# Kernel tuning notes

Hardware: AMD Instinct MI355X
Metric: run time of the kernel (lower is better)

Reference implementation:

```python
import jax, jax.numpy as jnp
import numpy as np

EMBED = 1024
HEADS = 16
HEAD_DIM = EMBED // HEADS
SCALE = HEAD_DIM ** -0.5


def setup_inputs() -> dict:
    key = jax.random.key(0)
    ks = jax.random.split(key, 11)
    B, S, D = 2, 2048, EMBED
    s = D ** -0.5
    return {
        "Q": jax.random.normal(ks[0], (B, S, D), jnp.float32),
        "K": jax.random.normal(ks[1], (B, S, D), jnp.float32),
        "V": jax.random.normal(ks[2], (B, S, D), jnp.float32),
        "Wq": jax.random.normal(ks[3], (D, D), jnp.float32) * s,
        "bq": jax.random.normal(ks[4], (D,), jnp.float32) * 0.01,
        "Wk": jax.random.normal(ks[5], (D, D), jnp.float32) * s,
        "bk": jax.random.normal(ks[6], (D,), jnp.float32) * 0.01,
        "Wv": jax.random.normal(ks[7], (D, D), jnp.float32) * s,
        "bv": jax.random.normal(ks[8], (D,), jnp.float32) * 0.01,
        "Wo": jax.random.normal(ks[9], (D, D), jnp.float32) * s,
        "bo": jax.random.normal(ks[10], (D,), jnp.float32) * 0.01,
    }


def reference(Q, K, V, Wq, bq, Wk, bk, Wv, bv, Wo, bo):
    N, S, D = Q.shape
    H, Hd = HEADS, HEAD_DIM
    # linear projections (x @ W + b), then split heads: [N, S, H, Hd]
    q = (Q @ Wq + bq).reshape(N, S, H, Hd)
    k = (K @ Wk + bk).reshape(N, S, H, Hd)
    v = (V @ Wv + bv).reshape(N, S, H, Hd)
    # scaled dot-product attention, full [N,H,S,S] scores as in the original
    energy = jnp.einsum('nqhd,nkhd->nhqk', q, k) * SCALE
    attn = jax.nn.softmax(energy, axis=3)
    out = jnp.einsum('nhql,nlhd->nqhd', attn, v).reshape(N, S, D)
    return out @ Wo + bo
```

## Files before the change

kernel.cpp:

```cpp
#include <hip/hip_runtime.h>
#include <cstdint>


typedef _Float16 h8 __attribute__((ext_vector_type(8)));
typedef float f4 __attribute__((ext_vector_type(4)));
typedef float f16v __attribute__((ext_vector_type(16)));
typedef unsigned int u32x4 __attribute__((ext_vector_type(4)));
typedef const unsigned int __attribute__((address_space(1)))* gp1_t;
typedef unsigned int __attribute__((address_space(3)))* lp3_t;

__device__ __forceinline__ void gld_lds16(const void* g, const void* l) {
  __builtin_amdgcn_global_load_lds((gp1_t)(uintptr_t)g,
                                   (lp3_t)(unsigned int)(uintptr_t)l, 16, 0, 0);
}
__device__ __forceinline__ unsigned pkh(float a, float b) {
  return __builtin_bit_cast(unsigned, __builtin_amdgcn_cvt_pkrtz(a, b));
}
__device__ __forceinline__ void plswap(unsigned& a, unsigned& b) {
  asm volatile("v_permlane32_swap_b32 %0, %1" : "+v"(a), "+v"(b));
}


__global__ void cvt_x3(const float* __restrict__ a, const float* __restrict__ b,
                       const float* __restrict__ c, _Float16* __restrict__ out) {
  const int z = blockIdx.z;
  const float* in = (z == 0) ? a : (z == 1) ? b : c;
  _Float16* o = out + (size_t)z * 4194304;
  const int i = (blockIdx.x * 256 + threadIdx.x) * 8;
  float4 u = *(const float4*)(in + i);
  float4 w = *(const float4*)(in + i + 4);
  h8 r = {(_Float16)u.x, (_Float16)u.y, (_Float16)u.z, (_Float16)u.w,
          (_Float16)w.x, (_Float16)w.y, (_Float16)w.z, (_Float16)w.w};
  *(h8*)(o + i) = r;
}

__global__ void cvt_w4(const float* __restrict__ wq, const float* __restrict__ wk,
                       const float* __restrict__ wv, const float* __restrict__ wo,
                       _Float16* __restrict__ WT) {
  const int z = blockIdx.z;
  const float* W = (z == 0) ? wq : (z == 1) ? wk : (z == 2) ? wv : wo;
  _Float16* o = WT + (size_t)z * 1048576;
  const int k = blockIdx.x * 256 + threadIdx.x;
  const int n0 = blockIdx.y * 4;
  float4 w = *(const float4*)(W + (size_t)k * 1024 + n0);
  o[(size_t)(n0 + 0) * 1024 + k] = (_Float16)w.x;
  o[(size_t)(n0 + 1) * 1024 + k] = (_Float16)w.y;
  o[(size_t)(n0 + 2) * 1024 + k] = (_Float16)w.z;
  o[(size_t)(n0 + 3) * 1024 + k] = (_Float16)w.w;
}


__device__ __forceinline__ void gemm_core(const _Float16* __restrict__ A,
                                          const _Float16* __restrict__ Bt,
                                          const float* __restrict__ bias,
                                          _Float16* __restrict__ out16,
                                          float* __restrict__ out32,
                                          int N, int K, int mode) {
  __shared__ _Float16 As[8192];
  __shared__ _Float16 Bs[8192];
  const int tid = threadIdx.x;
  const int wave = tid >> 6, lane = tid & 63;
  const int lg = lane >> 4, ll = lane & 15;
  const int wr = wave >> 1, wc = wave & 1;
  const int row0 = blockIdx.y * 128, col0 = blockIdx.x * 128;
  f4 acc[4][4] = {};
  const int nkt = K >> 6;
  for (int kt = 0; kt < nkt; ++kt) {
#pragma unroll
    for (int rr = 0; rr < 4; ++rr) {
      const int idx = rr * 256 + tid;
      const int r = idx >> 3, g = idx & 7;
      const int lb = (rr * 256 + wave * 64) * 8;
      gld_lds16(A + (size_t)(row0 + r) * K + kt * 64 + g * 8, &As[lb]);
      gld_lds16(Bt + (size_t)(col0 + r) * K + kt * 64 + g * 8, &Bs[lb]);
    }
    __syncthreads();
#pragma unroll
    for (int kk = 0; kk < 2; ++kk) {
      h8 af[4], bf[4];
#pragma unroll
      for (int mi = 0; mi < 4; ++mi)
        af[mi] = *(const h8*)&As[(wr * 64 + mi * 16 + ll) * 64 + kk * 32 + lg * 8];
#pragma unroll
      for (int ni = 0; ni < 4; ++ni)
        bf[ni] = *(const h8*)&Bs[(wc * 64 + ni * 16 + ll) * 64 + kk * 32 + lg * 8];
#pragma unroll
      for (int mi = 0; mi < 4; ++mi)
#pragma unroll
        for (int ni = 0; ni < 4; ++ni)
          acc[mi][ni] = __builtin_amdgcn_mfma_f32_16x16x32_f16(af[mi], bf[ni],
                                                               acc[mi][ni], 0, 0, 0);
    }
    __syncthreads();
  }
#pragma unroll
  for (int ni = 0; ni < 4; ++ni) {
    const int c = col0 + wc * 64 + ni * 16 + ll;
    const float bv = bias[c];
#pragma unroll
    for (int mi = 0; mi < 4; ++mi) {
#pragma unroll
      for (int i = 0; i < 4; ++i) {
        const int r = row0 + wr * 64 + mi * 16 + lg * 4 + i;
        const float val = acc[mi][ni][i] + bv;
        if (mode == 0) {
          const int b = r >> 11, s = r & 2047, h = c >> 6, hd = c & 63;
          out16[((size_t)((b * 16 + h) * 2048 + s)) * 64 + hd] = (_Float16)val;
        } else {
          out32[(size_t)r * N + c] = val;
        }
      }
    }
  }
}

__global__ __launch_bounds__(256) void gemm_qkv(const _Float16* __restrict__ X16,
                                                const _Float16* __restrict__ WT,
                                                const float* __restrict__ bq,
                                                const float* __restrict__ bk,
                                                const float* __restrict__ bv,
                                                _Float16* __restrict__ qkv16) {
  const int z = blockIdx.z;
  gemm_core(X16 + (size_t)z * 4194304, WT + (size_t)z * 1048576,
            (z == 0) ? bq : (z == 1) ? bk : bv, qkv16 + (size_t)z * 4194304,
            nullptr, 1024, 1024, 0);
}

__global__ __launch_bounds__(256) void gemm_out_k(const _Float16* __restrict__ A16,
                                                  const _Float16* __restrict__ WoT,
                                                  const float* __restrict__ bo,
                                                  float* __restrict__ out) {
  gemm_core(A16, WoT, bo, nullptr, out, 1024, 1024, 1);
}


#define STAGE_K(BUF, KT)                                                      \
  do {                                                                        \
    _Pragma("unroll") for (int rr = 0; rr < 2; ++rr) {                        \
      const int idx_ = rr * 256 + tid;                                        \
      const int r_ = idx_ >> 3, g_ = idx_ & 7;                                \
      gld_lds16(kbp + (size_t)((KT) * 64 + r_) * 64 + ((g_ ^ (r_ & 7)) * 8),  \
                &Ks[BUF][rr * 2048 + wave * 512]);                            \
    }                                                                         \
  } while (0)

#define LOAD_V(KT, VA, VC)                                                    \
  do {                                                                        \
    const _Float16* vp_ = vbp + (size_t)((KT) * 64 + vkey0) * 64 + vhd0;      \
    VA = *(const uint4*)vp_;                                                  \
    VC = *(const uint4*)(vp_ + 64);                                           \
  } while (0)

#define WRITE_V(BUF, VA, VC)                                                  \
  do {                                                                        \
    const unsigned short* pa_ = (const unsigned short*)&VA;                   \
    const unsigned short* pc_ = (const unsigned short*)&VC;                   \
    _Pragma("unroll") for (int j_ = 0; j_ < 8; ++j_) {                        \
      const int row_ = vhd0 + j_;                                             \
      const int hi_ = row_ * 64 + (((vkey0 >> 3) ^ (row_ & 7)) << 3) + (vkey0 & 7); \
      *(unsigned int*)&Vt[BUF][hi_] =                                         \
          (unsigned)pa_[j_] | ((unsigned)pc_[j_] << 16);                      \
    }                                                                         \
  } while (0)

#define PV_STEP(SX, PP, KBP)                                                  \
  do {                                                                        \
    unsigned wA = pkh(SX[(PP) + 0], SX[(PP) + 1]);                            \
    unsigned wB = pkh(SX[(PP) + 2], SX[(PP) + 3]);                            \
    unsigned wC = pkh(SX[(PP) + 4], SX[(PP) + 5]);                            \
    unsigned wD = pkh(SX[(PP) + 6], SX[(PP) + 7]);                            \
    plswap(wA, wC);                                                           \
    plswap(wB, wD);                                                           \
    u32x4 afu = {wA, wB, wC, wD};                                             \
    h8 af = __builtin_bit_cast(h8, afu);                                      \
    const int sw_ = (((KBP) * 2 + hi) ^ (l31 & 7)) << 3;                      \
    h8 vf0 = *(const h8*)&Vt[cur][l31 * 64 + sw_];                            \
    h8 vf1 = *(const h8*)&Vt[cur][(32 + l31) * 64 + sw_];                     \
    acc0 = __builtin_amdgcn_mfma_f32_32x32x16_f16(af, vf0, acc0, 0, 0, 0);    \
    acc1 = __builtin_amdgcn_mfma_f32_32x32x16_f16(af, vf1, acc1, 0, 0, 0);    \
  } while (0)

__global__ __launch_bounds__(256, 2) void attn_kernel(
    const _Float16* __restrict__ q16, const _Float16* __restrict__ k16,
    const _Float16* __restrict__ v16, _Float16* __restrict__ aout) {
  __shared__ _Float16 Ks[2][4096];
  __shared__ _Float16 Vt[2][4096];
  __shared__ float Fb[4][32];
  const int tid = threadIdx.x;
  const int wave = tid >> 6, lane = tid & 63;
  const int l31 = lane & 31, hi = lane >> 5;
  const int bh = blockIdx.x, qb = blockIdx.y;
  const int q0w = qb * 128 + wave * 32;
  const _Float16* qbp = q16 + (size_t)bh * 131072;
  const _Float16* kbp = k16 + (size_t)bh * 131072;
  const _Float16* vbp = v16 + (size_t)bh * 131072;
  const int vkey0 = (tid & 31) * 2, vhd0 = (tid >> 5) * 8;

  h8 qf0 = *(const h8*)(qbp + (size_t)(q0w + l31) * 64 + 0 + hi * 8);
  h8 qf1 = *(const h8*)(qbp + (size_t)(q0w + l31) * 64 + 16 + hi * 8);
  h8 qf2 = *(const h8*)(qbp + (size_t)(q0w + l31) * 64 + 32 + hi * 8);
  h8 qf3 = *(const h8*)(qbp + (size_t)(q0w + l31) * 64 + 48 + hi * 8);

  f16v acc0 = {}, acc1 = {};
  float mval = -1e30f, lsum = 0.f;
  const float C = 0.125f * 1.44269504089f;

  {
    uint4 va, vc;
    STAGE_K(0, 0);
    LOAD_V(0, va, vc);
    WRITE_V(0, va, vc);
  }
  __syncthreads();

  int cur = 0;
  for (int kt = 0; kt < 32; ++kt) {
    uint4 va, vc;
    const bool pre = (kt + 1 < 32);
    if (pre) { STAGE_K(cur ^ 1, kt + 1); LOAD_V(kt + 1, va, vc); }

    f16v s0 = {}, s1 = {};
#pragma unroll
    for (int kc = 0; kc < 4; ++kc) {
      const int sw = ((kc * 2 + hi) ^ (l31 & 7)) << 3;
      h8 k0 = *(const h8*)&Ks[cur][l31 * 64 + sw];
      h8 k1 = *(const h8*)&Ks[cur][(32 + l31) * 64 + sw];
      h8 qf = (kc == 0) ? qf0 : (kc == 1) ? qf1 : (kc == 2) ? qf2 : qf3;
      s0 = __builtin_amdgcn_mfma_f32_32x32x16_f16(k0, qf, s0, 0, 0, 0);
      s1 = __builtin_amdgcn_mfma_f32_32x32x16_f16(k1, qf, s1, 0, 0, 0);
    }

    float t[8];
#pragma unroll
    for (int j = 0; j < 8; ++j)
      t[j] = fmaxf(fmaxf(s0[j], s0[j + 8]), fmaxf(s1[j], s1[j + 8]));
    float pm = fmaxf(fmaxf(fmaxf(t[0], t[1]), fmaxf(t[2], t[3])),
                     fmaxf(fmaxf(t[4], t[5]), fmaxf(t[6], t[7])));
    pm = fmaxf(pm, __shfl_xor(pm, 32));
    const float pms = pm * C;

    if (__any(pms > mval + 8.0f)) {
      const float mnew = fmaxf(mval, pms);
      const float f = __builtin_amdgcn_exp2f(mval - mnew);
      mval = mnew;
      lsum *= f;
      Fb[wave][l31] = f;
      const f4 fr0 = *(const f4*)&Fb[wave][0 + 4 * hi];
      const f4 fr1 = *(const f4*)&Fb[wave][8 + 4 * hi];
      const f4 fr2 = *(const f4*)&Fb[wave][16 + 4 * hi];
      const f4 fr3 = *(const f4*)&Fb[wave][24 + 4 * hi];
#pragma unroll
      for (int r = 0; r < 16; ++r) {
        const float fx = (r < 4 ? fr0 : r < 8 ? fr1 : r < 12 ? fr2 : fr3)[r & 3];
        acc0[r] *= fx;
        acc1[r] *= fx;
      }
    }

#pragma unroll
    for (int r = 0; r < 16; ++r) {
      s0[r] = __builtin_amdgcn_exp2f(s0[r] * C - mval);
      s1[r] = __builtin_amdgcn_exp2f(s1[r] * C - mval);
    }
    float z[8];
#pragma unroll
    for (int j = 0; j < 8; ++j)
      z[j] = (s0[j] + s0[j + 8]) + (s1[j] + s1[j + 8]);
    lsum += ((z[0] + z[1]) + (z[2] + z[3])) + ((z[4] + z[5]) + (z[6] + z[7]));

    PV_STEP(s0, 0, 0);
    PV_STEP(s0, 8, 1);
    PV_STEP(s1, 0, 2);
    PV_STEP(s1, 8, 3);

    if (pre) WRITE_V(cur ^ 1, va, vc);
    __syncthreads();
    cur ^= 1;
  }

  lsum += __shfl_xor(lsum, 32);
  const float inv = 1.0f / lsum;
  Fb[wave][l31] = inv;
  const f4 ir0 = *(const f4*)&Fb[wave][0 + 4 * hi];
  const f4 ir1 = *(const f4*)&Fb[wave][8 + 4 * hi];
  const f4 ir2 = *(const f4*)&Fb[wave][16 + 4 * hi];
  const f4 ir3 = *(const f4*)&Fb[wave][24 + 4 * hi];
  const int b = bh >> 4, h = bh & 15;
#pragma unroll
  for (int r = 0; r < 16; ++r) {
    const float fx = (r < 4 ? ir0 : r < 8 ? ir1 : r < 12 ? ir2 : ir3)[r & 3];
    const int srow = q0w + (r & 3) + 8 * (r >> 2) + 4 * hi;
    _Float16* op = aout + ((size_t)(b * 2048 + srow)) * 1024 + h * 64 + l31;
    op[0] = (_Float16)(acc0[r] * fx);
    op[32] = (_Float16)(acc1[r] * fx);
  }
}


extern "C" void kernel_launch(void* const* d_in, const int* in_sizes, int n_in,
                              void* d_out, int out_size, void* d_ws, size_t ws_size,
                              hipStream_t stream) {
  const float* Q  = (const float*)d_in[0];
  const float* K  = (const float*)d_in[1];
  const float* V  = (const float*)d_in[2];
  const float* Wq = (const float*)d_in[3];
  const float* bq = (const float*)d_in[4];
  const float* Wk = (const float*)d_in[5];
  const float* bk = (const float*)d_in[6];
  const float* Wv = (const float*)d_in[7];
  const float* bv = (const float*)d_in[8];
  const float* Wo = (const float*)d_in[9];
  const float* bo = (const float*)d_in[10];

  _Float16* H      = (_Float16*)d_ws;
  _Float16* X16    = H;
  _Float16* WT     = H + 12582912;
  _Float16* qkv16  = H + 16777216;
  _Float16* aout16 = H + 29360128;
  float* out = (float*)d_out;

  cvt_x3<<<dim3(2048, 1, 3), 256, 0, stream>>>(Q, K, V, X16);
  cvt_w4<<<dim3(4, 256, 4), 256, 0, stream>>>(Wq, Wk, Wv, Wo, WT);
  gemm_qkv<<<dim3(8, 32, 3), 256, 0, stream>>>(X16, WT, bq, bk, bv, qkv16);
  attn_kernel<<<dim3(32, 16), 256, 0, stream>>>(qkv16, qkv16 + 4194304,
                                                qkv16 + 8388608, aout16);
  gemm_out_k<<<dim3(8, 32), 256, 0, stream>>>(aout16, WT + 3145728, bo, out);
}
```

Baseline: 152.3 us.

## Double-buffer GEMM tiles with swizzled LDS, and reshape attention blocks with XCD mapping

The GEMM core now double-buffers its A/B tiles in LDS, prefetching the next k-tile while computing the current one, and applies an XOR swizzle to the tile layout to avoid LDS bank conflicts. Both GEMM kernels gain an occupancy hint of 2 blocks. The attention kernel shrinks to 128 threads covering 64 query rows, launches a 1D grid whose block index is remapped so each XCD handles a contiguous set of heads for L2 locality, and adds s_setprio around the MFMA sections. The cost is twice the LDS per GEMM block and more K/V reload traffic per query row in attention.

```diff
diff --git a/kernel.cpp b/kernel.cpp
--- a/kernel.cpp
+++ b/kernel.cpp
@@ -8,6 +8,8 @@
 typedef unsigned int u32x4 __attribute__((ext_vector_type(4)));
 typedef const unsigned int __attribute__((address_space(1)))* gp1_t;
 typedef unsigned int __attribute__((address_space(3)))* lp3_t;
+
+#define FSWZ(r) ((((r) ^ ((r) >> 3))) & 7)
 
 __device__ __forceinline__ void gld_lds16(const void* g, const void* l) {
   __builtin_amdgcn_global_load_lds((gp1_t)(uintptr_t)g,
@@ -50,14 +52,27 @@
 }
 
 
+#define G_STAGE(BUF, KT)                                                       \
+  do {                                                                         \
+    _Pragma("unroll") for (int rr_ = 0; rr_ < 4; ++rr_) {                      \
+      const int idx_ = rr_ * 256 + tid;                                        \
+      const int r_ = idx_ >> 3, g_ = idx_ & 7;                                 \
+      const int lb_ = (rr_ * 256 + wave * 64) * 8;                             \
+      gld_lds16(A + (size_t)(row0 + r_) * K + (KT) * 64 + (g_ ^ FSWZ(r_)) * 8, \
+                &As[BUF][lb_]);                                                \
+      gld_lds16(Bt + (size_t)(col0 + r_) * K + (KT) * 64 + (g_ ^ FSWZ(r_)) * 8,\
+                &Bs[BUF][lb_]);                                                \
+    }                                                                          \
+  } while (0)
+
 __device__ __forceinline__ void gemm_core(const _Float16* __restrict__ A,
                                           const _Float16* __restrict__ Bt,
                                           const float* __restrict__ bias,
                                           _Float16* __restrict__ out16,
                                           float* __restrict__ out32,
                                           int N, int K, int mode) {
-  __shared__ _Float16 As[8192];
-  __shared__ _Float16 Bs[8192];
+  __shared__ _Float16 As[2][8192];
+  __shared__ _Float16 Bs[2][8192];
   const int tid = threadIdx.x;
   const int wave = tid >> 6, lane = tid & 63;
   const int lg = lane >> 4, ll = lane & 15;
@@ -65,25 +80,24 @@
   const int row0 = blockIdx.y * 128, col0 = blockIdx.x * 128;
   f4 acc[4][4] = {};
   const int nkt = K >> 6;
+  G_STAGE(0, 0);
+  __syncthreads();
+  int cur = 0;
   for (int kt = 0; kt < nkt; ++kt) {
-#pragma unroll
-    for (int rr = 0; rr < 4; ++rr) {
-      const int idx = rr * 256 + tid;
-      const int r = idx >> 3, g = idx & 7;
-      const int lb = (rr * 256 + wave * 64) * 8;
-      gld_lds16(A + (size_t)(row0 + r) * K + kt * 64 + g * 8, &As[lb]);
-      gld_lds16(Bt + (size_t)(col0 + r) * K + kt * 64 + g * 8, &Bs[lb]);
-    }
-    __syncthreads();
+    if (kt + 1 < nkt) G_STAGE(cur ^ 1, kt + 1);
 #pragma unroll
     for (int kk = 0; kk < 2; ++kk) {
       h8 af[4], bf[4];
 #pragma unroll
-      for (int mi = 0; mi < 4; ++mi)
-        af[mi] = *(const h8*)&As[(wr * 64 + mi * 16 + ll) * 64 + kk * 32 + lg * 8];
-#pragma unroll
-      for (int ni = 0; ni < 4; ++ni)
-        bf[ni] = *(const h8*)&Bs[(wc * 64 + ni * 16 + ll) * 64 + kk * 32 + lg * 8];
+      for (int mi = 0; mi < 4; ++mi) {
+        const int r = wr * 64 + mi * 16 + ll;
+        af[mi] = *(const h8*)&As[cur][r * 64 + (((kk * 4 + lg) ^ FSWZ(r)) << 3)];
+      }
+#pragma unroll
+      for (int ni = 0; ni < 4; ++ni) {
+        const int r = wc * 64 + ni * 16 + ll;
+        bf[ni] = *(const h8*)&Bs[cur][r * 64 + (((kk * 4 + lg) ^ FSWZ(r)) << 3)];
+      }
 #pragma unroll
       for (int mi = 0; mi < 4; ++mi)
 #pragma unroll
@@ -92,6 +106,7 @@
                                                                acc[mi][ni], 0, 0, 0);
     }
     __syncthreads();
+    cur ^= 1;
   }
 #pragma unroll
   for (int ni = 0; ni < 4; ++ni) {
@@ -114,52 +129,60 @@
   }
 }
 
-__global__ __launch_bounds__(256) void gemm_qkv(const _Float16* __restrict__ X16,
-                                                const _Float16* __restrict__ WT,
-                                                const float* __restrict__ bq,
-                                                const float* __restrict__ bk,
-                                                const float* __restrict__ bv,
-                                                _Float16* __restrict__ qkv16) {
+__global__ __launch_bounds__(256, 2) void gemm_qkv(const _Float16* __restrict__ X16,
+                                                   const _Float16* __restrict__ WT,
+                                                   const float* __restrict__ bq,
+                                                   const float* __restrict__ bk,
+                                                   const float* __restrict__ bv,
+                                                   _Float16* __restrict__ qkv16) {
   const int z = blockIdx.z;
   gemm_core(X16 + (size_t)z * 4194304, WT + (size_t)z * 1048576,
             (z == 0) ? bq : (z == 1) ? bk : bv, qkv16 + (size_t)z * 4194304,
             nullptr, 1024, 1024, 0);
 }
 
-__global__ __launch_bounds__(256) void gemm_out_k(const _Float16* __restrict__ A16,
-                                                  const _Float16* __restrict__ WoT,
-                                                  const float* __restrict__ bo,
-                                                  float* __restrict__ out) {
+__global__ __launch_bounds__(256, 2) void gemm_out_k(const _Float16* __restrict__ A16,
+                                                     const _Float16* __restrict__ WoT,
+                                                     const float* __restrict__ bo,
+                                                     float* __restrict__ out) {
   gemm_core(A16, WoT, bo, nullptr, out, 1024, 1024, 1);
 }
 
 
 #define STAGE_K(BUF, KT)                                                      \
   do {                                                                        \
-    _Pragma("unroll") for (int rr = 0; rr < 2; ++rr) {                        \
-      const int idx_ = rr * 256 + tid;                                        \
+    _Pragma("unroll") for (int rr_ = 0; rr_ < 4; ++rr_) {                     \
+      const int idx_ = rr_ * 128 + tid;                                       \
       const int r_ = idx_ >> 3, g_ = idx_ & 7;                                \
-      gld_lds16(kbp + (size_t)((KT) * 64 + r_) * 64 + ((g_ ^ (r_ & 7)) * 8),  \
-                &Ks[BUF][rr * 2048 + wave * 512]);                            \
+      gld_lds16(kbp + (size_t)((KT) * 64 + r_) * 64 + ((g_ ^ FSWZ(r_)) * 8),  \
+                &Ks[BUF][(rr_ * 128 + wave * 64) * 8]);                       \
     }                                                                         \
   } while (0)
 
-#define LOAD_V(KT, VA, VC)                                                    \
+#define LOAD_V(KT, VA, VB, VC, VD)                                            \
   do {                                                                        \
     const _Float16* vp_ = vbp + (size_t)((KT) * 64 + vkey0) * 64 + vhd0;      \
     VA = *(const uint4*)vp_;                                                  \
+    VB = *(const uint4*)(vp_ + 32);                                           \
     VC = *(const uint4*)(vp_ + 64);                                           \
-  } while (0)
-
-#define WRITE_V(BUF, VA, VC)                                                  \
+    VD = *(const uint4*)(vp_ + 96);                                           \
+  } while (0)
+
+#define WRITE_V(BUF, VA, VB, VC, VD)                                          \
   do {                                                                        \
     const unsigned short* pa_ = (const unsigned short*)&VA;                   \
+    const unsigned short* pb_ = (const unsigned short*)&VB;                   \
     const unsigned short* pc_ = (const unsigned short*)&VC;                   \
+    const unsigned short* pd_ = (const unsigned short*)&VD;                   \
     _Pragma("unroll") for (int j_ = 0; j_ < 8; ++j_) {                        \
-      const int row_ = vhd0 + j_;                                             \
-      const int hi_ = row_ * 64 + (((vkey0 >> 3) ^ (row_ & 7)) << 3) + (vkey0 & 7); \
-      *(unsigned int*)&Vt[BUF][hi_] =                                         \
+      const int r1_ = vhd0 + j_;                                              \
+      *(unsigned*)&Vt[BUF][r1_ * 64 + (((vkey0 >> 3) ^ FSWZ(r1_)) << 3) +     \
+                           (vkey0 & 7)] =                                     \
           (unsigned)pa_[j_] | ((unsigned)pc_[j_] << 16);                      \
+      const int r2_ = vhd0 + 32 + j_;                                         \
+      *(unsigned*)&Vt[BUF][r2_ * 64 + (((vkey0 >> 3) ^ FSWZ(r2_)) << 3) +     \
+                           (vkey0 & 7)] =                                     \
+          (unsigned)pb_[j_] | ((unsigned)pd_[j_] << 16);                      \
     }                                                                         \
   } while (0)
 
@@ -173,24 +196,28 @@
     plswap(wB, wD);                                                           \
     u32x4 afu = {wA, wB, wC, wD};                                             \
     h8 af = __builtin_bit_cast(h8, afu);                                      \
-    const int sw_ = (((KBP) * 2 + hi) ^ (l31 & 7)) << 3;                      \
-    h8 vf0 = *(const h8*)&Vt[cur][l31 * 64 + sw_];                            \
-    h8 vf1 = *(const h8*)&Vt[cur][(32 + l31) * 64 + sw_];                     \
+    const int c_ = (KBP) * 2 + hi;                                            \
+    h8 vf0 = *(const h8*)&Vt[cur][l31 * 64 + ((c_ ^ FSWZ(l31)) << 3)];        \
+    h8 vf1 = *(const h8*)&Vt[cur][(32 + l31) * 64 +                           \
+                                  ((c_ ^ FSWZ(32 + l31)) << 3)];              \
     acc0 = __builtin_amdgcn_mfma_f32_32x32x16_f16(af, vf0, acc0, 0, 0, 0);    \
     acc1 = __builtin_amdgcn_mfma_f32_32x32x16_f16(af, vf1, acc1, 0, 0, 0);    \
   } while (0)
 
-__global__ __launch_bounds__(256, 2) void attn_kernel(
+__global__ __launch_bounds__(128, 2) void attn_kernel(
     const _Float16* __restrict__ q16, const _Float16* __restrict__ k16,
     const _Float16* __restrict__ v16, _Float16* __restrict__ aout) {
   __shared__ _Float16 Ks[2][4096];
   __shared__ _Float16 Vt[2][4096];
-  __shared__ float Fb[4][32];
+  __shared__ float Fb[2][32];
   const int tid = threadIdx.x;
   const int wave = tid >> 6, lane = tid & 63;
   const int l31 = lane & 31, hi = lane >> 5;
-  const int bh = blockIdx.x, qb = blockIdx.y;
-  const int q0w = qb * 128 + wave * 32;
+  const int blk = blockIdx.x;
+  const int xcd = blk & 7, j = blk >> 3;
+  const int bh = xcd * 4 + (j >> 5);
+  const int qb = j & 31;
+  const int q0w = qb * 64 + wave * 32;
   const _Float16* qbp = q16 + (size_t)bh * 131072;
   const _Float16* kbp = k16 + (size_t)bh * 131072;
   const _Float16* vbp = v16 + (size_t)bh * 131072;
@@ -205,35 +232,34 @@
   float mval = -1e30f, lsum = 0.f;
   const float C = 0.125f * 1.44269504089f;
 
-  {
-    uint4 va, vc;
-    STAGE_K(0, 0);
-    LOAD_V(0, va, vc);
-    WRITE_V(0, va, vc);
-  }
+  uint4 va, vb, vc, vd;
+  STAGE_K(0, 0);
+  LOAD_V(0, va, vb, vc, vd);
+  WRITE_V(0, va, vb, vc, vd);
   __syncthreads();
 
   int cur = 0;
   for (int kt = 0; kt < 32; ++kt) {
-    uint4 va, vc;
     const bool pre = (kt + 1 < 32);
-    if (pre) { STAGE_K(cur ^ 1, kt + 1); LOAD_V(kt + 1, va, vc); }
+    if (pre) { STAGE_K(cur ^ 1, kt + 1); LOAD_V(kt + 1, va, vb, vc, vd); }
 
     f16v s0 = {}, s1 = {};
+    __builtin_amdgcn_s_setprio(1);
 #pragma unroll
     for (int kc = 0; kc < 4; ++kc) {
-      const int sw = ((kc * 2 + hi) ^ (l31 & 7)) << 3;
-      h8 k0 = *(const h8*)&Ks[cur][l31 * 64 + sw];
-      h8 k1 = *(const h8*)&Ks[cur][(32 + l31) * 64 + sw];
+      const int c = kc * 2 + hi;
+      h8 k0 = *(const h8*)&Ks[cur][l31 * 64 + ((c ^ FSWZ(l31)) << 3)];
+      h8 k1 = *(const h8*)&Ks[cur][(32 + l31) * 64 + ((c ^ FSWZ(32 + l31)) << 3)];
       h8 qf = (kc == 0) ? qf0 : (kc == 1) ? qf1 : (kc == 2) ? qf2 : qf3;
       s0 = __builtin_amdgcn_mfma_f32_32x32x16_f16(k0, qf, s0, 0, 0, 0);
       s1 = __builtin_amdgcn_mfma_f32_32x32x16_f16(k1, qf, s1, 0, 0, 0);
     }
+    __builtin_amdgcn_s_setprio(0);
 
     float t[8];
 #pragma unroll
-    for (int j = 0; j < 8; ++j)
-      t[j] = fmaxf(fmaxf(s0[j], s0[j + 8]), fmaxf(s1[j], s1[j + 8]));
+    for (int j2 = 0; j2 < 8; ++j2)
+      t[j2] = fmaxf(fmaxf(s0[j2], s0[j2 + 8]), fmaxf(s1[j2], s1[j2 + 8]));
     float pm = fmaxf(fmaxf(fmaxf(t[0], t[1]), fmaxf(t[2], t[3])),
                      fmaxf(fmaxf(t[4], t[5]), fmaxf(t[6], t[7])));
     pm = fmaxf(pm, __shfl_xor(pm, 32));
@@ -264,16 +290,18 @@
     }
     float z[8];
 #pragma unroll
-    for (int j = 0; j < 8; ++j)
-      z[j] = (s0[j] + s0[j + 8]) + (s1[j] + s1[j + 8]);
+    for (int j2 = 0; j2 < 8; ++j2)
+      z[j2] = (s0[j2] + s0[j2 + 8]) + (s1[j2] + s1[j2 + 8]);
     lsum += ((z[0] + z[1]) + (z[2] + z[3])) + ((z[4] + z[5]) + (z[6] + z[7]));
 
+    __builtin_amdgcn_s_setprio(1);
     PV_STEP(s0, 0, 0);
     PV_STEP(s0, 8, 1);
     PV_STEP(s1, 0, 2);
     PV_STEP(s1, 8, 3);
-
-    if (pre) WRITE_V(cur ^ 1, va, vc);
+    __builtin_amdgcn_s_setprio(0);
+
+    if (pre) WRITE_V(cur ^ 1, va, vb, vc, vd);
     __syncthreads();
     cur ^= 1;
   }
@@ -322,7 +350,7 @@
   cvt_x3<<<dim3(2048, 1, 3), 256, 0, stream>>>(Q, K, V, X16);
   cvt_w4<<<dim3(4, 256, 4), 256, 0, stream>>>(Wq, Wk, Wv, Wo, WT);
   gemm_qkv<<<dim3(8, 32, 3), 256, 0, stream>>>(X16, WT, bq, bk, bv, qkv16);
-  attn_kernel<<<dim3(32, 16), 256, 0, stream>>>(qkv16, qkv16 + 4194304,
-                                                qkv16 + 8388608, aout16);
+  attn_kernel<<<dim3(1024), 128, 0, stream>>>(qkv16, qkv16 + 4194304,
+                                              qkv16 + 8388608, aout16);
   gemm_out_k<<<dim3(8, 32), 256, 0, stream>>>(aout16, WT + 3145728, bo, out);
 }
```

Result: faster. 144.9 us (-4.9%).
